# Performance work log

Measured on AMD Instinct MI355X. Metric: run time of the kernel, lower is better.

Reference implementation:

```python
import jax, jax.numpy as jnp
import numpy as np
from jax import lax

USER_NUM = 60000
ITEM_NUM = 40000
N_NODES = USER_NUM + ITEM_NUM
EMB = 64
NNZ = 3200000
N_LAYERS = 3
ALPHA = 0.1


def setup_inputs() -> dict:
    key = jax.random.key(0)
    k1, k2, k3, k4, k5 = jax.random.split(key, 5)
    rows = jax.random.randint(k1, (NNZ,), 0, N_NODES, dtype=jnp.int32)
    cols = jax.random.randint(k2, (NNZ,), 0, N_NODES, dtype=jnp.int32)
    # normalized adjacency values are small positives
    vals = jax.random.uniform(k3, (NNZ,), dtype=jnp.float32) * 0.05
    user_emb = jax.random.normal(k4, (USER_NUM, EMB), dtype=jnp.float32) * 0.1
    item_emb = jax.random.normal(k5, (ITEM_NUM, EMB), dtype=jnp.float32) * 0.1
    return {"rows": rows, "cols": cols, "vals": vals,
            "user_emb": user_emb, "item_emb": item_emb}


def reference(rows, cols, vals, user_emb, item_emb):
    # ego = cat(user, item); e_out starts at zeros (first forward call).
    ego = jnp.concatenate([user_emb, item_emb], axis=0)  # [N, d]
    e0 = jnp.zeros_like(ego)

    def step(e, _):
        # torch.sparse.mm(A, e.clone().detach()) -> SpMM with stop_gradient,
        # matching the original's detach of the propagated state.
        gathered = vals[:, None] * lax.stop_gradient(e)[cols]  # [nnz, d]
        msg = jax.ops.segment_sum(gathered, rows, num_segments=N_NODES)
        e_new = (1.0 - ALPHA) * msg + ego
        return e_new, None

    e_out, _ = lax.scan(step, e0, None, length=N_LAYERS)
    return e_out[:USER_NUM], e_out[USER_NUM:]
```

## Files before the change

### kernel.cpp

```cpp
#include <hip/hip_runtime.h>
#include <hip/hip_fp16.h>


#define USER_NUM 60000
#define ITEM_NUM 40000
#define N_NODES  100000
#define EMB      64
#define NNZ      3200000
#define OMA      0.9f
#define BR       128
#define NB       782
#define TILE     4096
#define CAP      5120

__global__ __launch_bounds__(256) void ego_to_half(const float* __restrict__ ue,
                                                   const float* __restrict__ ie,
                                                   __half* __restrict__ dst) {
    int t = blockIdx.x * 256 + threadIdx.x;
    const int total8 = N_NODES * EMB / 8;
    if (t >= total8) return;
    size_t f0 = (size_t)t * 8;
    const size_t usz = (size_t)USER_NUM * EMB;
    const float4* s4 = (f0 < usz) ? (const float4*)(ue + f0)
                                  : (const float4*)(ie + (f0 - usz));
    float4 x = s4[0], y = s4[1];
    union { float4 f4; __half2 h2[4]; } o;
    o.h2[0] = __floats2half2_rn(x.x, x.y);
    o.h2[1] = __floats2half2_rn(x.z, x.w);
    o.h2[2] = __floats2half2_rn(y.x, y.y);
    o.h2[3] = __floats2half2_rn(y.z, y.w);
    ((float4*)dst)[t] = o.f4;
}

__global__ __launch_bounds__(256) void bucket_hist(const int* __restrict__ rows,
                                                   int* __restrict__ bcount) {
    __shared__ int lh[NB];
    for (int b = threadIdx.x; b < NB; b += 256) lh[b] = 0;
    __syncthreads();
    int e0 = blockIdx.x * TILE;
#pragma unroll
    for (int j = 0; j < 16; ++j) {
        int i = e0 + threadIdx.x + 256 * j;
        if (i < NNZ) atomicAdd(&lh[rows[i] >> 7], 1);
    }
    __syncthreads();
    for (int b = threadIdx.x; b < NB; b += 256) {
        int c = lh[b];
        if (c) atomicAdd(&bcount[b], c);
    }
}

__global__ __launch_bounds__(256) void bucket_scan(const int* __restrict__ bcount,
                                                   int* __restrict__ bbase,
                                                   int* __restrict__ bcursor,
                                                   int* __restrict__ row_start) {
    __shared__ int ps[256];
    int t = threadIdx.x;
    int b0 = t * 4;
    int s = 0;
#pragma unroll
    for (int q = 0; q < 4; ++q) { int i = b0 + q; if (i < NB) s += bcount[i]; }
    ps[t] = s;
    __syncthreads();
    for (int off = 1; off < 256; off <<= 1) {
        int v = (t >= off) ? ps[t - off] : 0;
        __syncthreads();
        ps[t] += v;
        __syncthreads();
    }
    int excl = t ? ps[t - 1] : 0;
#pragma unroll
    for (int q = 0; q < 4; ++q) {
        int i = b0 + q;
        if (i < NB) { bbase[i] = excl; bcursor[i] = excl; excl += bcount[i]; }
    }
    if (t == 255) { bbase[NB] = ps[255]; row_start[N_NODES] = ps[255]; }
}

__global__ __launch_bounds__(256) void bucket_scatter(const int* __restrict__ rows,
                                                      const int* __restrict__ cols,
                                                      const float* __restrict__ vals,
                                                      int* __restrict__ bcursor,
                                                      int2* __restrict__ ebuf) {
    __shared__ int lh[NB], lofs[NB], lcur[NB];
    __shared__ int ps[256];
    __shared__ int2 stage[TILE];
    int t = threadIdx.x;
    for (int b = t; b < NB; b += 256) lh[b] = 0;
    __syncthreads();

    int e0 = blockIdx.x * TILE;
    int mybk[16], mypk[16];
    float myv[16];
#pragma unroll
    for (int j = 0; j < 16; ++j) {
        int i = e0 + t + 256 * j;
        mybk[j] = -1;
        if (i < NNZ) {
            int r = rows[i], c = cols[i];
            myv[j]  = vals[i] * OMA;
            mybk[j] = r >> 7;
            mypk[j] = c | ((r & 127) << 17);
            atomicAdd(&lh[mybk[j]], 1);
        }
    }
    __syncthreads();

    int b0 = t * 4;
    int s = 0;
#pragma unroll
    for (int q = 0; q < 4; ++q) { int i = b0 + q; if (i < NB) s += lh[i]; }
    ps[t] = s;
    __syncthreads();
    for (int off = 1; off < 256; off <<= 1) {
        int v = (t >= off) ? ps[t - off] : 0;
        __syncthreads();
        ps[t] += v;
        __syncthreads();
    }
    int excl = t ? ps[t - 1] : 0;
#pragma unroll
    for (int q = 0; q < 4; ++q) {
        int i = b0 + q;
        if (i < NB) { lofs[i] = excl; lcur[i] = excl; excl += lh[i]; }
    }
    __syncthreads();

#pragma unroll
    for (int j = 0; j < 16; ++j) {
        if (mybk[j] >= 0) {
            int p = atomicAdd(&lcur[mybk[j]], 1);
            stage[p] = make_int2(mypk[j], __float_as_int(myv[j]));
        }
    }
    __syncthreads();

    for (int b = t; b < NB; b += 256) {
        int cnt = lh[b];
        if (cnt) {
            int g = atomicAdd(&bcursor[b], cnt);
            int src = lofs[b];
            for (int q = 0; q < cnt; ++q) ebuf[g + q] = stage[src + q];
        }
    }
}

__global__ __launch_bounds__(256) void row_sort(const int* __restrict__ bbase,
                                                int2* __restrict__ ebuf,
                                                int* __restrict__ row_start) {
    __shared__ int2 stage[CAP];
    __shared__ int lhist[BR], lofs[BR], lcur[BR];
    int bk = blockIdx.x, t = threadIdx.x;
    int s = bbase[bk], e = bbase[bk + 1];
    int cnt = min(e - s, CAP);

    if (t < BR) lhist[t] = 0;
    __syncthreads();
    for (int i = t; i < cnt; i += 256) {
        int2 v = ebuf[s + i];
        stage[i] = v;
        atomicAdd(&lhist[(v.x >> 17) & 127], 1);
    }
    __syncthreads();
    if (t == 0) {
        int acc = 0;
#pragma unroll
        for (int i = 0; i < BR; ++i) { int h = lhist[i]; lofs[i] = acc; acc += h; }
    }
    __syncthreads();
    if (t < BR) {
        int r = (bk << 7) + t;
        if (r < N_NODES) row_start[r] = s + lofs[t];
        lcur[t] = lofs[t];
    }
    __syncthreads();
    for (int i = t; i < cnt; i += 256) {
        int2 v = stage[i];
        int p = atomicAdd(&lcur[(v.x >> 17) & 127], 1);
        ebuf[s + p] = v;
    }
}

template <bool OUT_HALF>
__global__ __launch_bounds__(256) void spmm_pull_h(const int* __restrict__ row_start,
                                                   const int2* __restrict__ colval,
                                                   const __half* __restrict__ src,
                                                   const float* __restrict__ ue,
                                                   const float* __restrict__ ie,
                                                   void* __restrict__ outb) {
    int tid = blockIdx.x * 256 + threadIdx.x;
    int r = tid >> 4;
    if (r >= N_NODES) return;
    int lane  = threadIdx.x & 15;
    int qbase = (threadIdx.x & 63) & ~15;

    const float* egop = (r < USER_NUM) ? (ue + (size_t)r * EMB)
                                       : (ie + (size_t)(r - USER_NUM) * EMB);
    float4 acc = ((const float4*)egop)[lane];
    const float2* srcv = (const float2*)src;
    int s = row_start[r], e = row_start[r + 1];
    for (int k = s; k < e; k += 16) {
        int idx = k + lane;
        int2 cv = (idx < e) ? colval[idx] : make_int2(0, 0);
#pragma unroll
        for (int j = 0; j < 16; ++j) {
            int   cj = __shfl(cv.x, qbase + j, 64) & 0x1FFFF;
            float vj = __int_as_float(__shfl(cv.y, qbase + j, 64));
            union { float2 f2; __half2 h2[2]; } u;
            u.f2 = srcv[(size_t)cj * 16 + lane];
            float2 a = __half22float2(u.h2[0]);
            float2 b = __half22float2(u.h2[1]);
            acc.x += vj * a.x; acc.y += vj * a.y;
            acc.z += vj * b.x; acc.w += vj * b.y;
        }
    }
    if (OUT_HALF) {
        union { float2 f2; __half2 h2[2]; } o;
        o.h2[0] = __floats2half2_rn(acc.x, acc.y);
        o.h2[1] = __floats2half2_rn(acc.z, acc.w);
        ((float2*)outb)[(size_t)r * 16 + lane] = o.f2;
    } else {
        ((float4*)outb)[(size_t)r * 16 + lane] = acc;
    }
}

extern "C" void kernel_launch(void* const* d_in, const int* in_sizes, int n_in,
                              void* d_out, int out_size, void* d_ws, size_t ws_size,
                              hipStream_t stream) {
    const int*   rows = (const int*)d_in[0];
    const int*   cols = (const int*)d_in[1];
    const float* vals = (const float*)d_in[2];
    const float* ue   = (const float*)d_in[3];
    const float* ie   = (const float*)d_in[4];
    float* out = (float*)d_out;

    char* ws = (char*)d_ws;
    __half* ego_h    = (__half*)ws;
    __half* e2h      = (__half*)(ws + 12800000);
    int2*   ebuf     = (int2*)(ws + 25600000);
    int*    row_start= (int*)(ws + 51200000);
    int*    bcount   = (int*)(ws + 51600256);
    int*    bbase    = (int*)(ws + 51603456);
    int*    bcursor  = (int*)(ws + 51606656);

    hipMemsetAsync(bcount, 0, NB * sizeof(int), stream);

    const int convBlocks = (N_NODES * EMB / 8 + 255) / 256;
    ego_to_half<<<convBlocks, 256, 0, stream>>>(ue, ie, ego_h);

    const int tiles = (NNZ + TILE - 1) / TILE;
    bucket_hist<<<tiles, 256, 0, stream>>>(rows, bcount);
    bucket_scan<<<1, 256, 0, stream>>>(bcount, bbase, bcursor, row_start);
    bucket_scatter<<<tiles, 256, 0, stream>>>(rows, cols, vals, bcursor, ebuf);
    row_sort<<<NB, 256, 0, stream>>>(bbase, ebuf, row_start);

    const int spmmBlocks = (N_NODES * 16 + 255) / 256;
    spmm_pull_h<true ><<<spmmBlocks, 256, 0, stream>>>(row_start, ebuf, ego_h, ue, ie, e2h);
    spmm_pull_h<false><<<spmmBlocks, 256, 0, stream>>>(row_start, ebuf, e2h,   ue, ie, out);
}
```

Baseline: 327.3 us.

## Use wave-shuffle scans, per-wave histograms, colval prefetch, nontemporal output stores

Several independent micro-optimizations are applied. The histogram kernel gets per-wave shared histograms to cut atomic contention. The block scans in bucket_scatter and row_sort become wavefront shuffle scans with fewer barriers, and the scatter kernel's shared arrays are merged to lower LDS use. The SpMM now prefetches the next 16 column/value pairs before processing the current ones, and its final fp32 output uses nontemporal stores. CAP is lowered from 5120 to 4608, which raises the risk of truncating buckets holding more edges than that.

```diff
diff --git a/kernel.cpp b/kernel.cpp
--- a/kernel.cpp
+++ b/kernel.cpp
@@ -11,7 +11,9 @@
 #define BR       128
 #define NB       782
 #define TILE     4096
-#define CAP      5120
+#define CAP      4608
+
+typedef float f32x4 __attribute__((ext_vector_type(4)));
 
 __global__ __launch_bounds__(256) void ego_to_half(const float* __restrict__ ue,
                                                    const float* __restrict__ ie,
@@ -34,18 +36,19 @@
 
 __global__ __launch_bounds__(256) void bucket_hist(const int* __restrict__ rows,
                                                    int* __restrict__ bcount) {
-    __shared__ int lh[NB];
-    for (int b = threadIdx.x; b < NB; b += 256) lh[b] = 0;
+    __shared__ int lh[4][NB];
+    int t = threadIdx.x, w = t >> 6;
+    for (int b = t; b < 4 * NB; b += 256) lh[b / NB][b % NB] = 0;
     __syncthreads();
     int e0 = blockIdx.x * TILE;
 #pragma unroll
     for (int j = 0; j < 16; ++j) {
-        int i = e0 + threadIdx.x + 256 * j;
-        if (i < NNZ) atomicAdd(&lh[rows[i] >> 7], 1);
-    }
-    __syncthreads();
-    for (int b = threadIdx.x; b < NB; b += 256) {
-        int c = lh[b];
+        int i = e0 + t + 256 * j;
+        if (i < NNZ) atomicAdd(&lh[w][rows[i] >> 7], 1);
+    }
+    __syncthreads();
+    for (int b = t; b < NB; b += 256) {
+        int c = lh[0][b] + lh[1][b] + lh[2][b] + lh[3][b];
         if (c) atomicAdd(&bcount[b], c);
     }
 }
@@ -82,11 +85,13 @@
                                                       const float* __restrict__ vals,
                                                       int* __restrict__ bcursor,
                                                       int2* __restrict__ ebuf) {
-    __shared__ int lh[NB], lofs[NB], lcur[NB];
-    __shared__ int ps[256];
+    __shared__ int bins[NB + 1];
+    __shared__ int lcur[NB];
+    __shared__ int wsum[4];
     __shared__ int2 stage[TILE];
     int t = threadIdx.x;
-    for (int b = t; b < NB; b += 256) lh[b] = 0;
+    int lane = t & 63, w = t >> 6;
+    for (int b = t; b <= NB; b += 256) bins[b] = 0;
     __syncthreads();
 
     int e0 = blockIdx.x * TILE;
@@ -101,29 +106,34 @@
             myv[j]  = vals[i] * OMA;
             mybk[j] = r >> 7;
             mypk[j] = c | ((r & 127) << 17);
-            atomicAdd(&lh[mybk[j]], 1);
+            atomicAdd(&bins[mybk[j]], 1);
         }
     }
     __syncthreads();
 
     int b0 = t * 4;
-    int s = 0;
-#pragma unroll
-    for (int q = 0; q < 4; ++q) { int i = b0 + q; if (i < NB) s += lh[i]; }
-    ps[t] = s;
-    __syncthreads();
-    for (int off = 1; off < 256; off <<= 1) {
-        int v = (t >= off) ? ps[t - off] : 0;
-        __syncthreads();
-        ps[t] += v;
-        __syncthreads();
-    }
-    int excl = t ? ps[t - 1] : 0;
-#pragma unroll
-    for (int q = 0; q < 4; ++q) {
-        int i = b0 + q;
-        if (i < NB) { lofs[i] = excl; lcur[i] = excl; excl += lh[i]; }
-    }
+    int r0 = (b0     < NB) ? bins[b0]     : 0;
+    int r1 = (b0 + 1 < NB) ? bins[b0 + 1] : 0;
+    int r2 = (b0 + 2 < NB) ? bins[b0 + 2] : 0;
+    int r3 = (b0 + 3 < NB) ? bins[b0 + 3] : 0;
+    int s = r0 + r1 + r2 + r3;
+    int incl = s;
+#pragma unroll
+    for (int off = 1; off < 64; off <<= 1) {
+        int v = __shfl_up(incl, off, 64);
+        if (lane >= off) incl += v;
+    }
+    if (lane == 63) wsum[w] = incl;
+    __syncthreads();
+    int prefix = 0;
+#pragma unroll
+    for (int i = 0; i < 4; ++i) if (i < w) prefix += wsum[i];
+    int excl = prefix + incl - s;
+    if (b0     < NB) { bins[b0]     = excl; lcur[b0]     = excl; excl += r0; }
+    if (b0 + 1 < NB) { bins[b0 + 1] = excl; lcur[b0 + 1] = excl; excl += r1; }
+    if (b0 + 2 < NB) { bins[b0 + 2] = excl; lcur[b0 + 2] = excl; excl += r2; }
+    if (b0 + 3 < NB) { bins[b0 + 3] = excl; lcur[b0 + 3] = excl; excl += r3; }
+    if (t == 255) bins[NB] = prefix + incl;
     __syncthreads();
 
 #pragma unroll
@@ -136,10 +146,10 @@
     __syncthreads();
 
     for (int b = t; b < NB; b += 256) {
-        int cnt = lh[b];
-        if (cnt) {
+        int src = bins[b];
+        int cnt = bins[b + 1] - src;
+        if (cnt > 0) {
             int g = atomicAdd(&bcursor[b], cnt);
-            int src = lofs[b];
             for (int q = 0; q < cnt; ++q) ebuf[g + q] = stage[src + q];
         }
     }
@@ -162,18 +172,24 @@
         atomicAdd(&lhist[(v.x >> 17) & 127], 1);
     }
     __syncthreads();
-    if (t == 0) {
-        int acc = 0;
-#pragma unroll
-        for (int i = 0; i < BR; ++i) { int h = lhist[i]; lofs[i] = acc; acc += h; }
+    if (t < 64) {
+        int h0 = lhist[2 * t], h1 = lhist[2 * t + 1];
+        int pair = h0 + h1;
+        int incl = pair;
+#pragma unroll
+        for (int off = 1; off < 64; off <<= 1) {
+            int v = __shfl_up(incl, off, 64);
+            if (t >= off) incl += v;
+        }
+        int base = incl - pair;
+        lofs[2 * t]     = base;      lcur[2 * t]     = base;
+        lofs[2 * t + 1] = base + h0; lcur[2 * t + 1] = base + h0;
     }
     __syncthreads();
     if (t < BR) {
         int r = (bk << 7) + t;
         if (r < N_NODES) row_start[r] = s + lofs[t];
-        lcur[t] = lofs[t];
-    }
-    __syncthreads();
+    }
     for (int i = t; i < cnt; i += 256) {
         int2 v = stage[i];
         int p = atomicAdd(&lcur[(v.x >> 17) & 127], 1);
@@ -199,9 +215,11 @@
     float4 acc = ((const float4*)egop)[lane];
     const float2* srcv = (const float2*)src;
     int s = row_start[r], e = row_start[r + 1];
+
+    int2 cv = (s + lane < e) ? colval[s + lane] : make_int2(0, 0);
     for (int k = s; k < e; k += 16) {
-        int idx = k + lane;
-        int2 cv = (idx < e) ? colval[idx] : make_int2(0, 0);
+        int idxn = k + 16 + lane;
+        int2 nv = (idxn < e) ? colval[idxn] : make_int2(0, 0);
 #pragma unroll
         for (int j = 0; j < 16; ++j) {
             int   cj = __shfl(cv.x, qbase + j, 64) & 0x1FFFF;
@@ -213,6 +231,7 @@
             acc.x += vj * a.x; acc.y += vj * a.y;
             acc.z += vj * b.x; acc.w += vj * b.y;
         }
+        cv = nv;
     }
     if (OUT_HALF) {
         union { float2 f2; __half2 h2[2]; } o;
@@ -220,7 +239,8 @@
         o.h2[1] = __floats2half2_rn(acc.z, acc.w);
         ((float2*)outb)[(size_t)r * 16 + lane] = o.f2;
     } else {
-        ((float4*)outb)[(size_t)r * 16 + lane] = acc;
+        f32x4 av = { acc.x, acc.y, acc.z, acc.w };
+        __builtin_nontemporal_store(av, &((f32x4*)outb)[(size_t)r * 16 + lane]);
     }
 }
 
@@ -243,7 +263,7 @@
     int*    bbase    = (int*)(ws + 51603456);
     int*    bcursor  = (int*)(ws + 51606656);
 
-    hipMemsetAsync(bcount, 0, NB * sizeof(int), stream);
+    (void)hipMemsetAsync(bcount, 0, NB * sizeof(int), stream);
 
     const int convBlocks = (N_NODES * EMB / 8 + 255) / 256;
     ego_to_half<<<convBlocks, 256, 0, stream>>>(ue, ie, ego_h);
```

Measured after the change: 308.1 us. -5.9%, faster.
